# Kernel tuning notes

Hardware: AMD Instinct MI355X
Metric: run time of the kernel (lower is better)

The kernel has to match this reference:

```python
import jax, jax.numpy as jnp
import numpy as np

B, S, HID, NH = 2, 2048, 1024, 16
HD = HID // NH

def setup_inputs() -> dict:
    key = jax.random.key(0)
    ks = jax.random.split(key, 9)
    s = 1.0 / np.sqrt(HID)
    return {
        "hidden_state": jax.random.normal(ks[0], (B, S, HID), jnp.float32),
        "Wq": jax.random.normal(ks[1], (HID, HID), jnp.float32) * s,
        "bq": jax.random.normal(ks[2], (HID,), jnp.float32) * 0.02,
        "Wk": jax.random.normal(ks[3], (HID, HID), jnp.float32) * s,
        "bk": jax.random.normal(ks[4], (HID,), jnp.float32) * 0.02,
        "Wv": jax.random.normal(ks[5], (HID, HID), jnp.float32) * s,
        "bv": jax.random.normal(ks[6], (HID,), jnp.float32) * 0.02,
        "Wo": jax.random.normal(ks[7], (HID, HID), jnp.float32) * s,
        "bo": jax.random.normal(ks[8], (HID,), jnp.float32) * 0.02,
    }

def _split_heads(x):
    # [B,S,HID] -> [B,NH,S,HD]
    b, s, _ = x.shape
    return x.reshape(b, s, NH, HD).transpose(0, 2, 1, 3)

def reference(hidden_state, Wq, bq, Wk, bk, Wv, bv, Wo, bo):
    # torch nn.Linear: y = x @ W.T + b
    q = _split_heads(hidden_state @ Wq.T + bq)
    k = _split_heads(hidden_state @ Wk.T + bk)
    v = _split_heads(hidden_state @ Wv.T + bv)
    scale = 1.0 / jnp.sqrt(jnp.asarray(HD, hidden_state.dtype))
    scores = jnp.einsum("bhqd,bhkd->bhqk", q, k) * scale
    probs = jax.nn.softmax(scores, axis=-1)
    out = jnp.einsum("bhqk,bhkd->bhqd", probs, v)  # [B,NH,S,HD]
    out = out.transpose(0, 2, 1, 3).reshape(hidden_state.shape[0], -1, NH * HD)
    return out @ Wo.T + bo
```

## Files before the change

kernel.cpp:

```cpp
#include <hip/hip_runtime.h>


#define S_LEN 2048
#define HID   1024
#define NHEAD 16
#define HDIM  64
#define M_TOT 4096
#define LOG2E 1.4426950408889634f

typedef __attribute__((ext_vector_type(8))) short bf16x8;
typedef __attribute__((ext_vector_type(4))) float f32x4;

static __device__ __forceinline__ float b2f(short s) {
  union { unsigned int u; float f; } v;
  v.u = ((unsigned int)(unsigned short)s) << 16;
  return v.f;
}
static __device__ __forceinline__ short f2b(float f) {
  union { unsigned int u; float f; } v; v.f = f;
  unsigned int r = (v.u + 0x7FFFu + ((v.u >> 16) & 1u)) >> 16;
  return (short)(unsigned short)r;
}
static __device__ __forceinline__ short f2b_fast(float f) {
  union { unsigned int u; float f; } v; v.f = f;
  return (short)(unsigned short)((v.u + 0x8000u) >> 16);
}
static __device__ __forceinline__ float fexp2(float x) { return exp2f(x); }

#define GLD_LDS16(g, l)                                                        \
  __builtin_amdgcn_global_load_lds(                                            \
      (const __attribute__((address_space(1))) void*)(g),                      \
      (__attribute__((address_space(3))) void*)(l), 16, 0, 0)

__global__ __launch_bounds__(256) void detect_kernel(
    const unsigned short* __restrict__ X16, int* __restrict__ flag)
{
  __shared__ int cnt;
  if (threadIdx.x == 0) cnt = 0;
  __syncthreads();
  int local = 0;
  for (int i = threadIdx.x; i < 16384; i += 256) {
    unsigned short u = X16[i];
    int e = (u >> 7) & 0xFF;
    if (u == 0 || (e >= 0x60 && e <= 0x9F)) local++;
  }
  atomicAdd(&cnt, local);
  __syncthreads();
  if (threadIdx.x == 0) *flag = (cnt < 15000) ? 1 : 0;
}

__global__ __launch_bounds__(256) void convert_all_kernel(
    const void* s0, const void* s1, const void* s2, const void* s3,
    const void* s4, const void* s5, const void* s6, const void* s7,
    const void* s8,
    short* d0, short* d1, short* d2, short* d3, short* d4,
    short* d5, short* d6, short* d7, short* d8,
    const int* __restrict__ flagp)
{
  const void* src; short* dst; int n;
  switch (blockIdx.y) {
    case 0: src = s0; dst = d0; n = M_TOT * HID; break;
    case 1: src = s1; dst = d1; n = HID * HID; break;
    case 2: src = s2; dst = d2; n = HID; break;
    case 3: src = s3; dst = d3; n = HID * HID; break;
    case 4: src = s4; dst = d4; n = HID; break;
    case 5: src = s5; dst = d5; n = HID * HID; break;
    case 6: src = s6; dst = d6; n = HID; break;
    case 7: src = s7; dst = d7; n = HID * HID; break;
    default: src = s8; dst = d8; n = HID; break;
  }
  const int f = *flagp;
  const long stride = (long)gridDim.x * 256 * 4;
  long i = ((long)blockIdx.x * 256 + threadIdx.x) * 4;
  if (f) {
    const float* sf = (const float*)src;
    for (; i < n; i += stride) {
      float4 v = *(const float4*)(sf + i);
      ushort4 o;
      o.x = (unsigned short)f2b(v.x); o.y = (unsigned short)f2b(v.y);
      o.z = (unsigned short)f2b(v.z); o.w = (unsigned short)f2b(v.w);
      *(ushort4*)(dst + i) = o;
    }
  } else {
    const short* ss = (const short*)src;
    for (; i < n; i += stride)
      *(uint2*)(dst + i) = *(const uint2*)(ss + i);
  }
}

static __device__ __forceinline__ void gemm_core_128x128(
    const short* __restrict__ A, const short* __restrict__ W,
    int bm, int n0, short* Alds, short* Wlds, f32x4 acc[4][4])
{
  const int t    = threadIdx.x;
  const int lane = t & 63;
  const int w    = t >> 6;
  const int wm   = w >> 1, wn = w & 1;
  const int quad = lane >> 4, l15 = lane & 15;

  const int srow = t >> 3;
  const int cg   = (t & 7) ^ (srow & 7);
  const short* Ag = A + (size_t)(bm + srow) * HID + cg * 8;
  const short* Wg = W + (size_t)(n0 + srow) * HID + cg * 8;

  for (int k0 = 0; k0 < HID; k0 += 64) {
    __syncthreads();
#pragma unroll
    for (int i = 0; i < 4; ++i) {
      GLD_LDS16(Ag + (size_t)i * 32 * HID + k0, Alds + i * 2048 + t * 8);
      GLD_LDS16(Wg + (size_t)i * 32 * HID + k0, Wlds + i * 2048 + t * 8);
    }
    __syncthreads();

    bf16x8 af[4][2], bfr[4][2];
#pragma unroll
    for (int mt = 0; mt < 4; ++mt)
#pragma unroll
      for (int ks = 0; ks < 2; ++ks)
        af[mt][ks] = *(const bf16x8*)(Alds + (wm * 64 + mt * 16 + l15) * 64 +
                                      (((ks * 4 + quad) ^ (l15 & 7)) * 8));
#pragma unroll
    for (int nt = 0; nt < 4; ++nt)
#pragma unroll
      for (int ks = 0; ks < 2; ++ks)
        bfr[nt][ks] = *(const bf16x8*)(Wlds + (wn * 64 + nt * 16 + l15) * 64 +
                                       (((ks * 4 + quad) ^ (l15 & 7)) * 8));
#pragma unroll
    for (int mt = 0; mt < 4; ++mt)
#pragma unroll
      for (int nt = 0; nt < 4; ++nt) {
        acc[mt][nt] = __builtin_amdgcn_mfma_f32_16x16x32_bf16(af[mt][0], bfr[nt][0], acc[mt][nt], 0, 0, 0);
        acc[mt][nt] = __builtin_amdgcn_mfma_f32_16x16x32_bf16(af[mt][1], bfr[nt][1], acc[mt][nt], 0, 0, 0);
      }
  }
}

__global__ __launch_bounds__(256) void gemm_qkv_kernel(
    const short* __restrict__ X,
    const short* __restrict__ Wq, const short* __restrict__ Wk, const short* __restrict__ Wv,
    const short* __restrict__ bq, const short* __restrict__ bk, const short* __restrict__ bv,
    short* __restrict__ Q, short* __restrict__ K, short* __restrict__ V)
{
  __shared__ short Alds[128 * 64];
  __shared__ short Wlds[128 * 64];
  const int which = blockIdx.y >> 3;
  const int n0    = (blockIdx.y & 7) * 128;
  const int bm    = blockIdx.x * 128;
  const short* W    = (which == 0) ? Wq : (which == 1) ? Wk : Wv;
  const short* bias = (which == 0) ? bq : (which == 1) ? bk : bv;

  f32x4 acc[4][4];
#pragma unroll
  for (int i = 0; i < 4; ++i)
#pragma unroll
    for (int j = 0; j < 4; ++j) acc[i][j] = (f32x4){0.f, 0.f, 0.f, 0.f};

  gemm_core_128x128(X, W, bm, n0, Alds, Wlds, acc);

  const int t = threadIdx.x, lane = t & 63, w = t >> 6;
  const int wm = w >> 1, wn = w & 1;
  const int quad = lane >> 4, l15 = lane & 15;
  const float qscale = 0.125f * LOG2E;
#pragma unroll
  for (int nt = 0; nt < 4; ++nt) {
    const int n = n0 + wn * 64 + nt * 16 + l15;
    const float bvv = b2f(bias[n]);
#pragma unroll
    for (int mt = 0; mt < 4; ++mt) {
#pragma unroll
      for (int r = 0; r < 4; ++r) {
        const int m = bm + wm * 64 + mt * 16 + quad * 4 + r;
        const float val = acc[mt][nt][r] + bvv;
        if (which == 0) {
          Q[(size_t)m * HID + n] = f2b(val * qscale);
        } else if (which == 1) {
          K[(size_t)m * HID + n] = f2b(val);
        } else {
          const int b = m >> 11, s = m & 2047;
          V[((size_t)(b * 1024 + n)) * 2048 + s] = f2b(val);
        }
      }
    }
  }
}

static __device__ __forceinline__ void gemm_core_128x64(
    const short* __restrict__ A, const short* __restrict__ W,
    int bm, int n0, short* Alds, short* Wlds, f32x4 acc[2][4])
{
  const int t    = threadIdx.x;
  const int lane = t & 63;
  const int w    = t >> 6;
  const int quad = lane >> 4, l15 = lane & 15;

  const int srow = t >> 3;
  const int cg   = (t & 7) ^ (srow & 7);
  const short* Ag = A + (size_t)(bm + srow) * HID + cg * 8;
  const short* Wg = W + (size_t)(n0 + srow) * HID + cg * 8;

  for (int k0 = 0; k0 < HID; k0 += 64) {
    __syncthreads();
#pragma unroll
    for (int i = 0; i < 4; ++i)
      GLD_LDS16(Ag + (size_t)i * 32 * HID + k0, Alds + i * 2048 + t * 8);
#pragma unroll
    for (int i = 0; i < 2; ++i)
      GLD_LDS16(Wg + (size_t)i * 32 * HID + k0, Wlds + i * 2048 + t * 8);
    __syncthreads();

    bf16x8 af[2][2], bfr[4][2];
#pragma unroll
    for (int mt = 0; mt < 2; ++mt)
#pragma unroll
      for (int ks = 0; ks < 2; ++ks)
        af[mt][ks] = *(const bf16x8*)(Alds + (w * 32 + mt * 16 + l15) * 64 +
                                      (((ks * 4 + quad) ^ (l15 & 7)) * 8));
#pragma unroll
    for (int nt = 0; nt < 4; ++nt)
#pragma unroll
      for (int ks = 0; ks < 2; ++ks)
        bfr[nt][ks] = *(const bf16x8*)(Wlds + (nt * 16 + l15) * 64 +
                                       (((ks * 4 + quad) ^ (l15 & 7)) * 8));
#pragma unroll
    for (int mt = 0; mt < 2; ++mt)
#pragma unroll
      for (int nt = 0; nt < 4; ++nt) {
        acc[mt][nt] = __builtin_amdgcn_mfma_f32_16x16x32_bf16(af[mt][0], bfr[nt][0], acc[mt][nt], 0, 0, 0);
        acc[mt][nt] = __builtin_amdgcn_mfma_f32_16x16x32_bf16(af[mt][1], bfr[nt][1], acc[mt][nt], 0, 0, 0);
      }
  }
}

__global__ __launch_bounds__(256) void gemm_o_kernel(
    const short* __restrict__ A, const short* __restrict__ W,
    const short* __restrict__ bias, void* __restrict__ out,
    const int* __restrict__ flagp)
{
  __shared__ short Alds[128 * 64];
  __shared__ short Wlds[64 * 64];
  const int n0 = blockIdx.y * 64;
  const int bm = blockIdx.x * 128;
  const int f32out = *flagp;

  f32x4 acc[2][4];
#pragma unroll
  for (int i = 0; i < 2; ++i)
#pragma unroll
    for (int j = 0; j < 4; ++j) acc[i][j] = (f32x4){0.f, 0.f, 0.f, 0.f};

  gemm_core_128x64(A, W, bm, n0, Alds, Wlds, acc);

  const int t = threadIdx.x, lane = t & 63, w = t >> 6;
  const int quad = lane >> 4, l15 = lane & 15;
#pragma unroll
  for (int nt = 0; nt < 4; ++nt) {
    const int n = n0 + nt * 16 + l15;
    const float bvv = b2f(bias[n]);
#pragma unroll
    for (int mt = 0; mt < 2; ++mt) {
#pragma unroll
      for (int r = 0; r < 4; ++r) {
        const int m = bm + w * 32 + mt * 16 + quad * 4 + r;
        const float val = acc[mt][nt][r] + bvv;
        const size_t idx = (size_t)m * HID + n;
        if (f32out) ((float*)out)[idx] = val;
        else        ((short*)out)[idx] = f2b(val);
      }
    }
  }
}

__global__ __launch_bounds__(256) void flash_attn_kernel(
    const short* __restrict__ Q, const short* __restrict__ K,
    const short* __restrict__ V, short* __restrict__ O)
{
  __shared__ short Kl0[64 * 64], Kl1[64 * 64];
  __shared__ short Vl0[64 * 64], Vl1[64 * 64];
  __shared__ short Pl[4 * 16 * 64];

  const int t    = threadIdx.x;
  const int lane = t & 63, w = t >> 6;
  const int quad = lane >> 4, l15 = lane & 15;
  const int qtile = blockIdx.x;
  const int bh    = blockIdx.y;
  const int b = bh >> 4, h = bh & 15;
  const int hoff = h * HDIM;

  const int qrow = b * S_LEN + qtile * 64 + w * 16 + l15;
  bf16x8 qf[2];
#pragma unroll
  for (int ks = 0; ks < 2; ++ks)
    qf[ks] = *(const bf16x8*)(Q + (size_t)qrow * HID + hoff + ks * 32 + quad * 8);

  f32x4 o[4], ol;
#pragma unroll
  for (int nt = 0; nt < 4; ++nt) o[nt] = (f32x4){0.f, 0.f, 0.f, 0.f};
  ol = (f32x4){0.f, 0.f, 0.f, 0.f};

  bf16x8 vones;
#pragma unroll
  for (int j = 0; j < 8; ++j) vones[j] = (short)0x3F80;

  short* myP = Pl + w * (16 * 64);
  const int srow = t >> 3;
  const int cg   = (t & 7) ^ (srow & 7);
  const short* Kg = K + (size_t)(b * S_LEN) * HID + hoff + cg * 8;
  const short* Vg = V + (size_t)(bh * HDIM) * S_LEN + cg * 8;

  auto stage = [&](short* dK, short* dV, int kv0) {
    GLD_LDS16(Kg + (size_t)(kv0 + srow) * HID,      dK + t * 8);
    GLD_LDS16(Kg + (size_t)(kv0 + 32 + srow) * HID, dK + 2048 + t * 8);
    GLD_LDS16(Vg + (size_t)srow * S_LEN + kv0,        dV + t * 8);
    GLD_LDS16(Vg + (size_t)(32 + srow) * S_LEN + kv0, dV + 2048 + t * 8);
  };

  auto step = [&](int it, const short* Kc, const short* Vc, short* Kn, short* Vn) {
    __syncthreads();
    if (it < 31) stage(Kn, Vn, (it + 1) * 64);

    f32x4 s[4];
#pragma unroll
    for (int kt = 0; kt < 4; ++kt) {
      s[kt] = (f32x4){0.f, 0.f, 0.f, 0.f};
#pragma unroll
      for (int ks = 0; ks < 2; ++ks) {
        bf16x8 kf = *(const bf16x8*)(Kc + (kt * 16 + l15) * 64 +
                                     (((ks * 4 + quad) ^ (l15 & 7)) * 8));
        s[kt] = __builtin_amdgcn_mfma_f32_16x16x32_bf16(qf[ks], kf, s[kt], 0, 0, 0);
      }
    }

#pragma unroll
    for (int kt = 0; kt < 4; ++kt)
#pragma unroll
      for (int r = 0; r < 4; ++r)
        myP[(quad * 4 + r) * 64 + (((kt * 2 + (l15 >> 3)) ^ quad) * 8) + (l15 & 7)] =
            f2b_fast(fexp2(s[kt][r]));

    bf16x8 pa[2];
#pragma unroll
    for (int ks = 0; ks < 2; ++ks)
      pa[ks] = *(const bf16x8*)(myP + l15 * 64 +
                                (((ks * 4 + quad) ^ ((l15 >> 2) & 3)) * 8));

#pragma unroll
    for (int nt = 0; nt < 4; ++nt) {
#pragma unroll
      for (int ks = 0; ks < 2; ++ks) {
        bf16x8 vf = *(const bf16x8*)(Vc + (nt * 16 + l15) * 64 +
                                     (((ks * 4 + quad) ^ (l15 & 7)) * 8));
        o[nt] = __builtin_amdgcn_mfma_f32_16x16x32_bf16(pa[ks], vf, o[nt], 0, 0, 0);
      }
    }
    ol = __builtin_amdgcn_mfma_f32_16x16x32_bf16(pa[0], vones, ol, 0, 0, 0);
    ol = __builtin_amdgcn_mfma_f32_16x16x32_bf16(pa[1], vones, ol, 0, 0, 0);
  };

  stage(Kl0, Vl0, 0);
#pragma unroll 1
  for (int it = 0; it < 32; it += 2) {
    step(it,     Kl0, Vl0, Kl1, Vl1);
    step(it + 1, Kl1, Vl1, Kl0, Vl0);
  }

  const int orow = b * S_LEN + qtile * 64 + w * 16 + quad * 4;
#pragma unroll
  for (int nt = 0; nt < 4; ++nt) {
    const int col = hoff + nt * 16 + l15;
#pragma unroll
    for (int r = 0; r < 4; ++r)
      O[(size_t)(orow + r) * HID + col] = f2b(o[nt][r] / ol[r]);
  }
}

extern "C" void kernel_launch(void* const* d_in, const int* in_sizes, int n_in,
                              void* d_out, int out_size, void* d_ws, size_t ws_size,
                              hipStream_t stream) {
  short* WS  = (short*)d_ws;
  const size_t M1 = 1024 * 1024;
  short* Xc  = WS;
  short* Wqc = WS + 4 * M1;
  short* Wkc = WS + 5 * M1;
  short* Wvc = WS + 6 * M1;
  short* Woc = WS + 7 * M1;
  short* bqc = WS + 8 * M1;
  short* bkc = bqc + 1024;
  short* bvc = bkc + 1024;
  short* boc = bvc + 1024;
  short* Qb  = WS + 9 * M1;
  short* Kb  = WS + 13 * M1;
  short* Vt  = WS + 17 * M1;
  short* An  = WS + 21 * M1;
  int*   flag = (int*)(WS + 25 * M1);

  detect_kernel<<<1, 256, 0, stream>>>((const unsigned short*)d_in[0], flag);

  convert_all_kernel<<<dim3(128, 9), 256, 0, stream>>>(
      d_in[0], d_in[1], d_in[2], d_in[3], d_in[4], d_in[5], d_in[6], d_in[7], d_in[8],
      Xc, Wqc, bqc, Wkc, bkc, Wvc, bvc, Woc, boc, flag);

  gemm_qkv_kernel<<<dim3(32, 24), 256, 0, stream>>>(
      Xc, Wqc, Wkc, Wvc, bqc, bkc, bvc, Qb, Kb, Vt);

  flash_attn_kernel<<<dim3(32, 32), 256, 0, stream>>>(Qb, Kb, Vt, An);

  gemm_o_kernel<<<dim3(32, 16), 256, 0, stream>>>(An, Woc, boc, d_out, flag);
}
```

Measured before the change: 240.4 us.

## Process two 16-row query tiles per wave in flash attention

Each wave now computes 32 query rows instead of 16. The K and V fragments read from LDS are shared across both row tiles, and the grid's query-tile dimension is halved. This cuts LDS and global traffic per unit of work. In exchange, register pressure rises, the P scratch buffer doubles, and there are half as many blocks to fill the GPU.

```diff
diff --git a/kernel.cpp b/kernel.cpp
--- a/kernel.cpp
+++ b/kernel.cpp
@@ -276,7 +276,7 @@
 {
   __shared__ short Kl0[64 * 64], Kl1[64 * 64];
   __shared__ short Vl0[64 * 64], Vl1[64 * 64];
-  __shared__ short Pl[4 * 16 * 64];
+  __shared__ short Pl[4 * 32 * 64];
 
   const int t    = threadIdx.x;
   const int lane = t & 63, w = t >> 6;
@@ -286,22 +286,28 @@
   const int b = bh >> 4, h = bh & 15;
   const int hoff = h * HDIM;
 
-  const int qrow = b * S_LEN + qtile * 64 + w * 16 + l15;
-  bf16x8 qf[2];
-#pragma unroll
-  for (int ks = 0; ks < 2; ++ks)
-    qf[ks] = *(const bf16x8*)(Q + (size_t)qrow * HID + hoff + ks * 32 + quad * 8);
-
-  f32x4 o[4], ol;
-#pragma unroll
-  for (int nt = 0; nt < 4; ++nt) o[nt] = (f32x4){0.f, 0.f, 0.f, 0.f};
-  ol = (f32x4){0.f, 0.f, 0.f, 0.f};
+  bf16x8 qf[2][2];
+#pragma unroll
+  for (int mt = 0; mt < 2; ++mt) {
+    const int qrow = b * S_LEN + qtile * 128 + w * 32 + mt * 16 + l15;
+#pragma unroll
+    for (int ks = 0; ks < 2; ++ks)
+      qf[mt][ks] = *(const bf16x8*)(Q + (size_t)qrow * HID + hoff + ks * 32 + quad * 8);
+  }
+
+  f32x4 o[2][4], ol[2];
+#pragma unroll
+  for (int mt = 0; mt < 2; ++mt) {
+#pragma unroll
+    for (int nt = 0; nt < 4; ++nt) o[mt][nt] = (f32x4){0.f, 0.f, 0.f, 0.f};
+    ol[mt] = (f32x4){0.f, 0.f, 0.f, 0.f};
+  }
 
   bf16x8 vones;
 #pragma unroll
   for (int j = 0; j < 8; ++j) vones[j] = (short)0x3F80;
 
-  short* myP = Pl + w * (16 * 64);
+  short* myP = Pl + w * (32 * 64);
   const int srow = t >> 3;
   const int cg   = (t & 7) ^ (srow & 7);
   const short* Kg = K + (size_t)(b * S_LEN) * HID + hoff + cg * 8;
@@ -318,30 +324,39 @@
     __syncthreads();
     if (it < 31) stage(Kn, Vn, (it + 1) * 64);
 
-    f32x4 s[4];
-#pragma unroll
-    for (int kt = 0; kt < 4; ++kt) {
-      s[kt] = (f32x4){0.f, 0.f, 0.f, 0.f};
-#pragma unroll
-      for (int ks = 0; ks < 2; ++ks) {
-        bf16x8 kf = *(const bf16x8*)(Kc + (kt * 16 + l15) * 64 +
-                                     (((ks * 4 + quad) ^ (l15 & 7)) * 8));
-        s[kt] = __builtin_amdgcn_mfma_f32_16x16x32_bf16(qf[ks], kf, s[kt], 0, 0, 0);
-      }
-    }
-
+    bf16x8 kf[4][2];
 #pragma unroll
     for (int kt = 0; kt < 4; ++kt)
 #pragma unroll
-      for (int r = 0; r < 4; ++r)
-        myP[(quad * 4 + r) * 64 + (((kt * 2 + (l15 >> 3)) ^ quad) * 8) + (l15 & 7)] =
-            f2b_fast(fexp2(s[kt][r]));
-
-    bf16x8 pa[2];
-#pragma unroll
-    for (int ks = 0; ks < 2; ++ks)
-      pa[ks] = *(const bf16x8*)(myP + l15 * 64 +
-                                (((ks * 4 + quad) ^ ((l15 >> 2) & 3)) * 8));
+      for (int ks = 0; ks < 2; ++ks)
+        kf[kt][ks] = *(const bf16x8*)(Kc + (kt * 16 + l15) * 64 +
+                                      (((ks * 4 + quad) ^ (l15 & 7)) * 8));
+
+#pragma unroll
+    for (int mt = 0; mt < 2; ++mt) {
+      f32x4 s[4];
+#pragma unroll
+      for (int kt = 0; kt < 4; ++kt) {
+        s[kt] = (f32x4){0.f, 0.f, 0.f, 0.f};
+        s[kt] = __builtin_amdgcn_mfma_f32_16x16x32_bf16(qf[mt][0], kf[kt][0], s[kt], 0, 0, 0);
+        s[kt] = __builtin_amdgcn_mfma_f32_16x16x32_bf16(qf[mt][1], kf[kt][1], s[kt], 0, 0, 0);
+      }
+      short* Pm = myP + mt * (16 * 64);
+#pragma unroll
+      for (int kt = 0; kt < 4; ++kt)
+#pragma unroll
+        for (int r = 0; r < 4; ++r)
+          Pm[(quad * 4 + r) * 64 + (((kt * 2 + (l15 >> 3)) ^ quad) * 8) + (l15 & 7)] =
+              f2b_fast(fexp2(s[kt][r]));
+    }
+
+    bf16x8 pa[2][2];
+#pragma unroll
+    for (int mt = 0; mt < 2; ++mt)
+#pragma unroll
+      for (int ks = 0; ks < 2; ++ks)
+        pa[mt][ks] = *(const bf16x8*)(myP + (mt * 16 + l15) * 64 +
+                                      (((ks * 4 + quad) ^ ((l15 >> 2) & 3)) * 8));
 
 #pragma unroll
     for (int nt = 0; nt < 4; ++nt) {
@@ -349,11 +364,15 @@
       for (int ks = 0; ks < 2; ++ks) {
         bf16x8 vf = *(const bf16x8*)(Vc + (nt * 16 + l15) * 64 +
                                      (((ks * 4 + quad) ^ (l15 & 7)) * 8));
-        o[nt] = __builtin_amdgcn_mfma_f32_16x16x32_bf16(pa[ks], vf, o[nt], 0, 0, 0);
-      }
-    }
-    ol = __builtin_amdgcn_mfma_f32_16x16x32_bf16(pa[0], vones, ol, 0, 0, 0);
-    ol = __builtin_amdgcn_mfma_f32_16x16x32_bf16(pa[1], vones, ol, 0, 0, 0);
+        o[0][nt] = __builtin_amdgcn_mfma_f32_16x16x32_bf16(pa[0][ks], vf, o[0][nt], 0, 0, 0);
+        o[1][nt] = __builtin_amdgcn_mfma_f32_16x16x32_bf16(pa[1][ks], vf, o[1][nt], 0, 0, 0);
+      }
+    }
+#pragma unroll
+    for (int mt = 0; mt < 2; ++mt) {
+      ol[mt] = __builtin_amdgcn_mfma_f32_16x16x32_bf16(pa[mt][0], vones, ol[mt], 0, 0, 0);
+      ol[mt] = __builtin_amdgcn_mfma_f32_16x16x32_bf16(pa[mt][1], vones, ol[mt], 0, 0, 0);
+    }
   };
 
   stage(Kl0, Vl0, 0);
@@ -363,13 +382,16 @@
     step(it + 1, Kl1, Vl1, Kl0, Vl0);
   }
 
-  const int orow = b * S_LEN + qtile * 64 + w * 16 + quad * 4;
-#pragma unroll
-  for (int nt = 0; nt < 4; ++nt) {
-    const int col = hoff + nt * 16 + l15;
-#pragma unroll
-    for (int r = 0; r < 4; ++r)
-      O[(size_t)(orow + r) * HID + col] = f2b(o[nt][r] / ol[r]);
+#pragma unroll
+  for (int mt = 0; mt < 2; ++mt) {
+    const int orow = b * S_LEN + qtile * 128 + w * 32 + mt * 16 + quad * 4;
+#pragma unroll
+    for (int nt = 0; nt < 4; ++nt) {
+      const int col = hoff + nt * 16 + l15;
+#pragma unroll
+      for (int r = 0; r < 4; ++r)
+        O[(size_t)(orow + r) * HID + col] = f2b(o[mt][nt][r] / ol[mt][r]);
+    }
   }
 }
 
@@ -402,7 +424,7 @@
   gemm_qkv_kernel<<<dim3(32, 24), 256, 0, stream>>>(
       Xc, Wqc, Wkc, Wvc, bqc, bkc, bvc, Qb, Kb, Vt);
 
-  flash_attn_kernel<<<dim3(32, 32), 256, 0, stream>>>(Qb, Kb, Vt, An);
+  flash_attn_kernel<<<dim3(16, 32), 256, 0, stream>>>(Qb, Kb, Vt, An);
 
   gemm_o_kernel<<<dim3(32, 16), 256, 0, stream>>>(An, Woc, boc, d_out, flag);
 }
```

Result: no change. 237.5 us (-1.2%).
